# Optimization experiments

Hardware: AMD Instinct MI355X
Metric: run time of the kernel (lower is better)

The kernel has to match this reference:

```python
import jax, jax.numpy as jnp
import numpy as np

B, L, H, S = 16, 2048, 1024, 32
P, N_ASP, N_RAT = 256, 8, 5


def _layernorm(x, scale, bias, eps=1e-5):
    mu = jnp.mean(x, axis=-1, keepdims=True)
    var = jnp.mean(jnp.square(x - mu), axis=-1, keepdims=True)
    return (x - mu) * jax.lax.rsqrt(var + eps) * scale + bias


def _bndl(x, ln_s, ln_b, W):
    # BnDropLin eval: LayerNorm -> (Dropout off) -> Linear(no bias)
    return _layernorm(x, ln_s, ln_b) @ W


def setup_inputs() -> dict:
    key = jax.random.key(0)
    ks = jax.random.split(key, 8)
    outputs = jax.random.normal(ks[0], (B, L, H), dtype=jnp.float32)
    mask = jnp.ones((B, L), dtype=jnp.float32)
    # p_index: binary sentence-boundary markers, exactly S per doc, min gap 2
    rng = np.random.default_rng(0)
    p = np.zeros((B, L), dtype=np.int32)
    for b in range(B):
        idx = np.sort(rng.choice(L // 2 - 1, size=S, replace=False)) * 2 + 1
        p[b, idx] = 1
    p_index = jnp.asarray(p)
    sc = 0.02
    params = dict(
        ln_a_s=jnp.ones((H,), jnp.float32), ln_a_b=jnp.zeros((H,), jnp.float32),
        W_a=jax.random.normal(ks[1], (H, P), jnp.float32) * sc,
        ln_s_s=jnp.ones((H,), jnp.float32), ln_s_b=jnp.zeros((H,), jnp.float32),
        W_s=jax.random.normal(ks[2], (H, P), jnp.float32) * sc,
        ln_asp_s=jnp.ones((P,), jnp.float32), ln_asp_b=jnp.zeros((P,), jnp.float32),
        W_asp=jax.random.normal(ks[3], (P, N_ASP + 1), jnp.float32) * sc,
        ln_se_s=jnp.ones((P,), jnp.float32), ln_se_b=jnp.zeros((P,), jnp.float32),
        W_se=jax.random.normal(ks[4], (P, N_RAT), jnp.float32) * sc,
    )
    return dict(outputs=outputs, mask=mask, p_index=p_index, n_sent=S, **params)


def _segment_means(proj, end, start):
    # proj: [B, L, P]; start/end: [B, S] token index ranges [start, end)
    c = jnp.concatenate([jnp.zeros_like(proj[:, :1]), jnp.cumsum(proj, axis=1)], axis=1)  # [B,L+1,P]
    s_end = jnp.take_along_axis(c, end[:, :, None], axis=1)
    s_beg = jnp.take_along_axis(c, start[:, :, None], axis=1)
    cnt = (end - start).astype(proj.dtype)[:, :, None]
    return (s_end - s_beg) / cnt  # [B, S, P]


def reference(outputs, mask, p_index, n_sent,
              ln_a_s, ln_a_b, W_a, ln_s_s, ln_s_b, W_s,
              ln_asp_s, ln_asp_b, W_asp, ln_se_s, ln_se_b, W_se):
    b, l, h = outputs.shape
    n_asp = W_asp.shape[1] - 1
    flat = outputs.reshape(-1, h)
    a_proj = jax.nn.gelu(_bndl(flat, ln_a_s, ln_a_b, W_a), approximate=False).reshape(b, l, -1)
    s_proj = jax.nn.gelu(_bndl(flat, ln_s_s, ln_s_b, W_s), approximate=False).reshape(b, l, -1)
    # sentence boundaries: positions of nonzeros (exactly n_sent per row)
    pos = jnp.where(p_index > 0, jnp.arange(l)[None, :], l)
    pi = jnp.sort(pos, axis=1)[:, :n_sent]                      # [B,S] boundary idx (exclusive end)
    start = jnp.concatenate([jnp.zeros_like(pi[:, :1]), pi[:, :-1] + 1], axis=1)
    a_sent = _segment_means(a_proj, pi, start)                  # [B,S,P]
    s_sent = _segment_means(s_proj, pi, start)                  # [B,S,P]
    a_flat = a_sent.reshape(b * n_sent, -1)
    s_flat = s_sent.reshape(b * n_sent, -1)
    aspect_dist = jax.nn.softmax(_bndl(a_flat, ln_asp_s, ln_asp_b, W_asp), axis=1)  # [N, n_asp+1]
    aw = aspect_dist[:, :n_asp]                                 # [N, n_asp]
    sent_bmm = aw[:, :, None] * s_flat[:, None, :]              # [N, n_asp, P]
    doc_sum = sent_bmm.reshape(b, n_sent, n_asp, -1).sum(axis=1)        # [B, n_asp, P]
    w_sum = aw.reshape(b, n_sent, n_asp).sum(axis=1)[:, :, None]        # [B, n_asp, 1]
    doc_emb = doc_sum / w_sum
    # shared sentiment head (ModuleList([m]*n_asp) aliases one module)
    result = _bndl(doc_emb, ln_se_s, ln_se_b, W_se)             # [B, n_asp, n_rat]
    aspect_doc = aspect_dist.reshape(b, n_sent, n_asp + 1)
    return (result, outputs, aspect_doc)
```

## Files before the change

### kernel.cpp

```cpp
#include <hip/hip_runtime.h>
#include <cstdint>
#include <cstddef>

#define B_   16
#define L_   2048
#define H_   1024
#define S_   32
#define P_   256
#define NASP 8
#define NRAT 5
#define M_   (B_*L_)
#define N_   (2*P_)

typedef unsigned short u16;
typedef __bf16 bf16;
typedef u16  u16x4  __attribute__((ext_vector_type(4)));
typedef u16  u16x8  __attribute__((ext_vector_type(8)));
typedef bf16 bf16x8 __attribute__((ext_vector_type(8)));
typedef float f32x4 __attribute__((ext_vector_type(4)));

__device__ __forceinline__ u16 f2b(float f){
  unsigned int u = __float_as_uint(f);
  u += 0x7FFFu + ((u >> 16) & 1u);
  return (u16)(u >> 16);
}
__device__ __forceinline__ float b2f(u16 v){
  return __uint_as_float(((unsigned int)v) << 16);
}

__device__ __forceinline__ float2 block_reduce2(float a, float b){
  __shared__ float sh[8];
  #pragma unroll
  for (int o = 32; o > 0; o >>= 1){
    a += __shfl_down(a, o, 64);
    b += __shfl_down(b, o, 64);
  }
  int w = threadIdx.x >> 6;
  if ((threadIdx.x & 63) == 0){ sh[w] = a; sh[w + 4] = b; }
  __syncthreads();
  float2 r;
  r.x = sh[0] + sh[1] + sh[2] + sh[3];
  r.y = sh[4] + sh[5] + sh[6] + sh[7];
  __syncthreads();
  return r;
}

__global__ void fold_k(const float* __restrict__ Wa, const float* __restrict__ Ws,
                       const float* __restrict__ sa, const float* __restrict__ ba,
                       const float* __restrict__ ss, const float* __restrict__ bs,
                       u16* __restrict__ WcT, float* __restrict__ biasc){
  int n = blockIdx.x;
  const float* W; const float* sc; const float* bi; int col;
  if (n < P_){ W = Wa; sc = sa; bi = ba; col = n; }
  else       { W = Ws; sc = ss; bi = bs; col = n - P_; }
  float bacc = 0.f;
  #pragma unroll
  for (int i = 0; i < 4; ++i){
    int k = threadIdx.x + i * 256;
    float w = W[(size_t)k * P_ + col];
    WcT[(size_t)n * H_ + k] = f2b(w * sc[k]);
    bacc += w * bi[k];
  }
  float2 r = block_reduce2(bacc, 0.f);
  if (threadIdx.x == 0) biasc[n] = r.x;
}

__global__ void markers_k(const int* __restrict__ p_index, int* __restrict__ pi){
  int b = blockIdx.x;
  int lane = threadIdx.x;
  int cnt = 0;
  for (int c = 0; c < L_ / 64; ++c){
    int pos = c * 64 + lane;
    bool f = p_index[(size_t)b * L_ + pos] > 0;
    unsigned long long m = __ballot(f);
    int before = __popcll(m & ((1ull << lane) - 1ull));
    if (f){
      int idx = cnt + before;
      if (idx < S_) pi[b * S_ + idx] = pos;
    }
    cnt += __popcll(m);
  }
}

__global__ void stats_xhat_k(const float* __restrict__ x, u16* __restrict__ xhat){
  int row = blockIdx.x;
  int t = threadIdx.x;
  float4 v = ((const float4*)(x + (size_t)row * H_))[t];
  float s  = v.x + v.y + v.z + v.w;
  float ss = v.x*v.x + v.y*v.y + v.z*v.z + v.w*v.w;
  float2 r = block_reduce2(s, ss);
  float mean = r.x * (1.f / H_);
  float var  = fmaxf(r.y * (1.f / H_) - mean * mean, 0.f);
  float rstd = rsqrtf(var + 1e-5f);
  u16x4 o;
  o[0] = f2b((v.x - mean) * rstd);
  o[1] = f2b((v.y - mean) * rstd);
  o[2] = f2b((v.z - mean) * rstd);
  o[3] = f2b((v.w - mean) * rstd);
  ((u16x4*)(xhat + (size_t)row * H_))[t] = o;
}

__global__ __launch_bounds__(256) void gemm_k(const u16* __restrict__ xhat,
                                              const u16* __restrict__ WcT,
                                              const float* __restrict__ biasc,
                                              u16* __restrict__ proj){
  __shared__ __align__(16) u16 As[128][40];
  __shared__ __align__(16) u16 Bs[64][40];
  int t = threadIdx.x;
  unsigned int l = blockIdx.x;
  unsigned int xcd  = l & 7;
  unsigned int slot = l >> 3;
  unsigned int ntile = slot & 7;
  unsigned int mtile = xcd * 32 + (slot >> 3);
  int nbase = ntile * 64;
  int mbase = mtile * 128;

  int rowA = t >> 2, chA = t & 3;
  const u16* arow0 = xhat + (size_t)(mbase + rowA) * H_;
  const u16* arow1 = xhat + (size_t)(mbase + rowA + 64) * H_;
  int nB = t >> 2, chB = t & 3;
  const u16* wrow = WcT + (size_t)(nbase + nB) * H_;

  f32x4 acc[2][4] = {};
  int w = t >> 6, lane = t & 63, quad = lane >> 4, l15 = lane & 15;

  for (int kk = 0; kk < H_; kk += 32){
    __syncthreads();
    *reinterpret_cast<u16x8*>(&As[rowA][chA * 8]) =
        *reinterpret_cast<const u16x8*>(arow0 + kk + chA * 8);
    *reinterpret_cast<u16x8*>(&As[rowA + 64][chA * 8]) =
        *reinterpret_cast<const u16x8*>(arow1 + kk + chA * 8);
    *reinterpret_cast<u16x8*>(&Bs[nB][chB * 8]) =
        *reinterpret_cast<const u16x8*>(wrow + kk + chB * 8);
    __syncthreads();

    bf16x8 af0 = *reinterpret_cast<const bf16x8*>(&As[w * 32 + l15][quad * 8]);
    bf16x8 af1 = *reinterpret_cast<const bf16x8*>(&As[w * 32 + 16 + l15][quad * 8]);
    #pragma unroll
    for (int in = 0; in < 4; ++in){
      bf16x8 bf = *reinterpret_cast<const bf16x8*>(&Bs[in * 16 + l15][quad * 8]);
      acc[0][in] = __builtin_amdgcn_mfma_f32_16x16x32_bf16(af0, bf, acc[0][in], 0, 0, 0);
      acc[1][in] = __builtin_amdgcn_mfma_f32_16x16x32_bf16(af1, bf, acc[1][in], 0, 0, 0);
    }
  }

  #pragma unroll
  for (int in = 0; in < 4; ++in){
    int col = nbase + in * 16 + l15;
    float bv = biasc[col];
    #pragma unroll
    for (int im = 0; im < 2; ++im){
      #pragma unroll
      for (int r = 0; r < 4; ++r){
        int rowg = mbase + w * 32 + im * 16 + quad * 4 + r;
        float vv = acc[im][in][r] + bv;
        float g = 0.5f * vv * (1.0f + erff(vv * 0.70710678118654752f));
        proj[(size_t)rowg * N_ + col] = f2b(g);
      }
    }
  }
}

__global__ __launch_bounds__(1024) void segmean_k(const u16* __restrict__ proj,
                                                  const int* __restrict__ pi,
                                                  float* __restrict__ sent){
  int b = blockIdx.x, j = blockIdx.y;
  int t = threadIdx.x;
  int rg   = t >> 6;
  int lane = t & 63;
  int end   = pi[b * S_ + j];
  int start = (j == 0) ? 0 : (pi[b * S_ + j - 1] + 1);
  end   = min(max(end, 0), L_);
  start = min(max(start, 0), end);
  int cnt = max(end - start, 1);
  float inv = 1.0f / (float)cnt;

  float s[8] = {};
  const u16* base = proj + ((size_t)b * L_ + start) * N_ + lane * 8;
  for (int r = rg; r < cnt; r += 16){
    u16x8 v = *reinterpret_cast<const u16x8*>(base + (size_t)r * N_);
    #pragma unroll
    for (int k = 0; k < 8; ++k) s[k] += b2f(v[k]);
  }

  __shared__ float sh[16][N_];
  #pragma unroll
  for (int k = 0; k < 8; ++k) sh[rg][lane * 8 + k] = s[k];
  __syncthreads();

  if (t < N_){
    float acc = 0.f;
    #pragma unroll
    for (int g = 0; g < 16; ++g) acc += sh[g][t];
    sent[((size_t)b * S_ + j) * N_ + t] = acc * inv;
  }
}

__global__ void aspect_k(const float* __restrict__ sent,
                         const float* __restrict__ lns, const float* __restrict__ lnb,
                         const float* __restrict__ Wasp,
                         float* __restrict__ out_adoc, float* __restrict__ aw){
  int sidx = blockIdx.x;
  int t = threadIdx.x;
  float a = sent[(size_t)sidx * N_ + t];
  float2 r = block_reduce2(a, a * a);
  float mean = r.x * (1.f / P_);
  float var  = fmaxf(r.y * (1.f / P_) - mean * mean, 0.f);
  float rstd = rsqrtf(var + 1e-5f);
  __shared__ float shv[P_];
  shv[t] = (a - mean) * rstd * lns[t] + lnb[t];
  __syncthreads();
  __shared__ float lg[NASP + 1];
  if (t < NASP + 1){
    float acc = 0.f;
    for (int p = 0; p < P_; ++p) acc += shv[p] * Wasp[p * (NASP + 1) + t];
    lg[t] = acc;
  }
  __syncthreads();
  __shared__ float pr[NASP + 1];
  if (t == 0){
    float m = lg[0];
    #pragma unroll
    for (int i = 1; i < NASP + 1; ++i) m = fmaxf(m, lg[i]);
    float s = 0.f;
    #pragma unroll
    for (int i = 0; i < NASP + 1; ++i){ float e = expf(lg[i] - m); pr[i] = e; s += e; }
    float is = 1.f / s;
    #pragma unroll
    for (int i = 0; i < NASP + 1; ++i) pr[i] *= is;
  }
  __syncthreads();
  if (t < NASP + 1) out_adoc[(size_t)sidx * (NASP + 1) + t] = pr[t];
  if (t < NASP)     aw[(size_t)sidx * NASP + t] = pr[t];
}

__global__ void result_k(const float* __restrict__ sent, const float* __restrict__ aw,
                         const float* __restrict__ lns, const float* __restrict__ lnb,
                         const float* __restrict__ Wse, float* __restrict__ out){
  int ba = blockIdx.x;
  int b = ba >> 3, a = ba & 7;
  int t = threadIdx.x;
  float acc = 0.f, wsum = 0.f;
  for (int s2 = 0; s2 < S_; ++s2){
    float w = aw[((size_t)(b * S_ + s2)) * NASP + a];
    acc  += w * sent[((size_t)(b * S_ + s2)) * N_ + P_ + t];
    wsum += w;
  }
  float d = acc / fmaxf(wsum, 1e-20f);
  float2 r = block_reduce2(d, d * d);
  float mean = r.x * (1.f / P_);
  float var  = fmaxf(r.y * (1.f / P_) - mean * mean, 0.f);
  float rstd = rsqrtf(var + 1e-5f);
  __shared__ float shv[P_];
  shv[t] = (d - mean) * rstd * lns[t] + lnb[t];
  __syncthreads();
  if (t < NRAT){
    float s = 0.f;
    for (int p = 0; p < P_; ++p) s += shv[p] * Wse[p * NRAT + t];
    out[(size_t)ba * NRAT + t] = s;
  }
}

__global__ void copy_k(const float4* __restrict__ src, float4* __restrict__ dst){
  size_t i = (size_t)blockIdx.x * 256 + threadIdx.x;
  dst[i] = src[i];
}

extern "C" void kernel_launch(void* const* d_in, const int* in_sizes, int n_in,
                              void* d_out, int out_size, void* d_ws, size_t ws_size,
                              hipStream_t stream) {
  const float* x        = (const float*)d_in[0];
  const int*   p_index  = (const int*)d_in[2];
  const float* ln_a_s   = (const float*)d_in[4];
  const float* ln_a_b   = (const float*)d_in[5];
  const float* W_a      = (const float*)d_in[6];
  const float* ln_s_s   = (const float*)d_in[7];
  const float* ln_s_b   = (const float*)d_in[8];
  const float* W_s      = (const float*)d_in[9];
  const float* ln_asp_s = (const float*)d_in[10];
  const float* ln_asp_b = (const float*)d_in[11];
  const float* W_asp    = (const float*)d_in[12];
  const float* ln_se_s  = (const float*)d_in[13];
  const float* ln_se_b  = (const float*)d_in[14];
  const float* W_se     = (const float*)d_in[15];

  float* out_result = (float*)d_out;
  float* out_echo   = out_result + 640;
  float* out_adoc   = out_echo + (size_t)M_ * H_;

  u16* proj = (u16*)out_echo;
  u16* xhat = proj + (size_t)M_ * N_;

  char* ws = (char*)d_ws;
  u16*   WcT   = (u16*)ws;   ws += (size_t)N_ * H_ * 2;
  float* biasc = (float*)ws; ws += (size_t)N_ * 4;
  int*   pi    = (int*)ws;   ws += (size_t)B_ * S_ * 4;
  float* sent  = (float*)ws; ws += (size_t)B_ * S_ * N_ * 4;
  float* aw    = (float*)ws; ws += (size_t)B_ * S_ * NASP * 4;

  fold_k<<<N_, 256, 0, stream>>>(W_a, W_s, ln_a_s, ln_a_b, ln_s_s, ln_s_b, WcT, biasc);
  markers_k<<<B_, 64, 0, stream>>>(p_index, pi);
  stats_xhat_k<<<M_, 256, 0, stream>>>(x, xhat);
  gemm_k<<<2048, 256, 0, stream>>>(xhat, WcT, biasc, proj);
  segmean_k<<<dim3(B_, S_), 1024, 0, stream>>>(proj, pi, sent);
  aspect_k<<<B_ * S_, 256, 0, stream>>>(sent, ln_asp_s, ln_asp_b, W_asp, out_adoc, aw);
  result_k<<<B_ * NASP, 256, 0, stream>>>(sent, aw, ln_se_s, ln_se_b, W_se, out_result);
  copy_k<<<(M_ * H_ / 4) / 256, 256, 0, stream>>>((const float4*)x, (float4*)out_echo);
}
```

Measured before the change: 406.9 us.

## Enlarge GEMM tile to 128x128 with direct global-to-LDS loads and XOR swizzle

Tiles the projection GEMM as 128x128 instead of 128x64, with a 2x2 wave layout and 4x4 MFMA accumulators per wave. This halves the grid and raises data reuse per LDS load. Operand tiles now go straight from global memory into LDS via global_load_lds, so the register round-trip is gone. An XOR swizzle on the 16-byte chunks replaces the padding to avoid bank conflicts. In exchange, each wave holds more registers and the grid has fewer blocks, which may lower occupancy.

```diff
diff --git a/kernel.cpp b/kernel.cpp
--- a/kernel.cpp
+++ b/kernel.cpp
@@ -26,6 +26,12 @@
 }
 __device__ __forceinline__ float b2f(u16 v){
   return __uint_as_float(((unsigned int)v) << 16);
+}
+
+__device__ __forceinline__ void gload_lds16(const u16* g, u16* l){
+  __builtin_amdgcn_global_load_lds(
+      (const __attribute__((address_space(1))) unsigned int*)g,
+      (__attribute__((address_space(3))) unsigned int*)l, 16, 0, 0);
 }
 
 __device__ __forceinline__ float2 block_reduce2(float a, float b){
@@ -104,58 +110,73 @@
                                               const u16* __restrict__ WcT,
                                               const float* __restrict__ biasc,
                                               u16* __restrict__ proj){
-  __shared__ __align__(16) u16 As[128][40];
-  __shared__ __align__(16) u16 Bs[64][40];
+  __shared__ __align__(16) u16 As[128 * 32];
+  __shared__ __align__(16) u16 Bs[128 * 32];
   int t = threadIdx.x;
   unsigned int l = blockIdx.x;
   unsigned int xcd  = l & 7;
   unsigned int slot = l >> 3;
-  unsigned int ntile = slot & 7;
-  unsigned int mtile = xcd * 32 + (slot >> 3);
-  int nbase = ntile * 64;
-  int mbase = mtile * 128;
-
-  int rowA = t >> 2, chA = t & 3;
-  const u16* arow0 = xhat + (size_t)(mbase + rowA) * H_;
-  const u16* arow1 = xhat + (size_t)(mbase + rowA + 64) * H_;
-  int nB = t >> 2, chB = t & 3;
-  const u16* wrow = WcT + (size_t)(nbase + nB) * H_;
-
-  f32x4 acc[2][4] = {};
-  int w = t >> 6, lane = t & 63, quad = lane >> 4, l15 = lane & 15;
+  int nbase = (int)(slot & 3) * 128;
+  int mbase = (int)(xcd * 32 + (slot >> 2)) * 128;
+
+  int w = t >> 6, lane = t & 63;
+  int wr = w >> 1, wc = w & 1;
+  int quad = lane >> 4, l15 = lane & 15;
+
+  int g = (lane & 3) ^ ((lane >> 3) & 3);
+  int r0 = (w * 2 + 0) * 16 + (lane >> 2);
+  int r1 = (w * 2 + 1) * 16 + (lane >> 2);
+  const u16* gA0 = xhat + (size_t)(mbase + r0) * H_ + g * 8;
+  const u16* gA1 = xhat + (size_t)(mbase + r1) * H_ + g * 8;
+  const u16* gB0 = WcT  + (size_t)(nbase + r0) * H_ + g * 8;
+  const u16* gB1 = WcT  + (size_t)(nbase + r1) * H_ + g * 8;
+  u16* lA0 = As + (w * 2 + 0) * 512;
+  u16* lA1 = As + (w * 2 + 1) * 512;
+  u16* lB0 = Bs + (w * 2 + 0) * 512;
+  u16* lB1 = Bs + (w * 2 + 1) * 512;
+
+  f32x4 acc[4][4] = {};
 
   for (int kk = 0; kk < H_; kk += 32){
     __syncthreads();
-    *reinterpret_cast<u16x8*>(&As[rowA][chA * 8]) =
-        *reinterpret_cast<const u16x8*>(arow0 + kk + chA * 8);
-    *reinterpret_cast<u16x8*>(&As[rowA + 64][chA * 8]) =
-        *reinterpret_cast<const u16x8*>(arow1 + kk + chA * 8);
-    *reinterpret_cast<u16x8*>(&Bs[nB][chB * 8]) =
-        *reinterpret_cast<const u16x8*>(wrow + kk + chB * 8);
+    gload_lds16(gA0 + kk, lA0);
+    gload_lds16(gA1 + kk, lA1);
+    gload_lds16(gB0 + kk, lB0);
+    gload_lds16(gB1 + kk, lB1);
     __syncthreads();
 
-    bf16x8 af0 = *reinterpret_cast<const bf16x8*>(&As[w * 32 + l15][quad * 8]);
-    bf16x8 af1 = *reinterpret_cast<const bf16x8*>(&As[w * 32 + 16 + l15][quad * 8]);
+    bf16x8 af[4], bfr[4];
+    #pragma unroll
+    for (int im = 0; im < 4; ++im){
+      int R = wr * 64 + im * 16 + l15;
+      int cq = quad ^ ((R >> 1) & 3);
+      af[im] = *reinterpret_cast<const bf16x8*>(&As[R * 32 + cq * 8]);
+    }
     #pragma unroll
     for (int in = 0; in < 4; ++in){
-      bf16x8 bf = *reinterpret_cast<const bf16x8*>(&Bs[in * 16 + l15][quad * 8]);
-      acc[0][in] = __builtin_amdgcn_mfma_f32_16x16x32_bf16(af0, bf, acc[0][in], 0, 0, 0);
-      acc[1][in] = __builtin_amdgcn_mfma_f32_16x16x32_bf16(af1, bf, acc[1][in], 0, 0, 0);
+      int R = wc * 64 + in * 16 + l15;
+      int cq = quad ^ ((R >> 1) & 3);
+      bfr[in] = *reinterpret_cast<const bf16x8*>(&Bs[R * 32 + cq * 8]);
     }
+    #pragma unroll
+    for (int im = 0; im < 4; ++im)
+      #pragma unroll
+      for (int in = 0; in < 4; ++in)
+        acc[im][in] = __builtin_amdgcn_mfma_f32_16x16x32_bf16(af[im], bfr[in], acc[im][in], 0, 0, 0);
   }
 
   #pragma unroll
   for (int in = 0; in < 4; ++in){
-    int col = nbase + in * 16 + l15;
+    int col = nbase + wc * 64 + in * 16 + l15;
     float bv = biasc[col];
     #pragma unroll
-    for (int im = 0; im < 2; ++im){
+    for (int im = 0; im < 4; ++im){
       #pragma unroll
       for (int r = 0; r < 4; ++r){
-        int rowg = mbase + w * 32 + im * 16 + quad * 4 + r;
+        int rowg = mbase + wr * 64 + im * 16 + quad * 4 + r;
         float vv = acc[im][in][r] + bv;
-        float g = 0.5f * vv * (1.0f + erff(vv * 0.70710678118654752f));
-        proj[(size_t)rowg * N_ + col] = f2b(g);
+        float gl = 0.5f * vv * (1.0f + erff(vv * 0.70710678118654752f));
+        proj[(size_t)rowg * N_ + col] = f2b(gl);
       }
     }
   }
@@ -301,7 +322,7 @@
   fold_k<<<N_, 256, 0, stream>>>(W_a, W_s, ln_a_s, ln_a_b, ln_s_s, ln_s_b, WcT, biasc);
   markers_k<<<B_, 64, 0, stream>>>(p_index, pi);
   stats_xhat_k<<<M_, 256, 0, stream>>>(x, xhat);
-  gemm_k<<<2048, 256, 0, stream>>>(xhat, WcT, biasc, proj);
+  gemm_k<<<1024, 256, 0, stream>>>(xhat, WcT, biasc, proj);
   segmean_k<<<dim3(B_, S_), 1024, 0, stream>>>(proj, pi, sent);
   aspect_k<<<B_ * S_, 256, 0, stream>>>(sent, ln_asp_s, ln_asp_b, W_asp, out_adoc, aw);
   result_k<<<B_ * NASP, 256, 0, stream>>>(sent, aw, ln_se_s, ln_se_b, W_se, out_result);
```

After: 405.9 us. Within noise of the previous version (-0.3%).
